# Kernel optimization log

Measured on AMD Instinct MI355X. Metric: run time of the kernel, lower is better.

The kernel has to match this reference:

```python
import jax, jax.numpy as jnp
import numpy as np

# Module hyperparameters (from init_kwargs)
LATENT = 1024
H = 16          # num query heads
HK = 4          # num key/value heads (GQA)
D = 64          # head_dim
CAUSAL = True
QKV_OUT = (3 * H + 2 * HK) * D  # 3584, as defined in the source module


def setup_inputs() -> dict:
    key = jax.random.key(0)
    k1, k2, k3 = jax.random.split(key, 3)
    B, S = 2, 2048
    x = jax.random.normal(k1, (B, S, LATENT), dtype=jnp.float32)
    # nn.Linear weights are [out_features, in_features]; scale like torch default init
    w_qkv = jax.random.normal(k2, (QKV_OUT, LATENT), dtype=jnp.float32) / np.sqrt(LATENT)
    w_out = jax.random.normal(k3, (LATENT, H * D), dtype=jnp.float32) / np.sqrt(H * D)
    return {"x": x, "w_qkv": w_qkv, "w_out": w_out}


def reference(x, w_qkv, w_out):
    B, S, _ = x.shape
    scale = 1.0 / np.sqrt(D).astype(np.float32)

    # Fused QKV projection: [B,S,(3H+2HK)*D]
    qkv = jnp.einsum('bsl,ol->bso', x, w_qkv)

    # Split: q takes H heads, k and v take HK heads each (GQA).
    # (The extra 2*H*D columns of the fused projection are allocated by the
    #  source module but unused by q/k/v, matching its layer sizing.)
    q = qkv[..., : H * D].reshape(B, S, H, D)
    k = qkv[..., H * D:(H + HK) * D].reshape(B, S, HK, D)
    v = qkv[..., (H + HK) * D:(H + 2 * HK) * D].reshape(B, S, HK, D)

    # Expand KV heads to match query heads (group factor H // HK)
    rep = H // HK
    k = jnp.repeat(k, rep, axis=2)  # [B,S,H,D]
    v = jnp.repeat(v, rep, axis=2)

    # Scaled dot-product attention
    scores = jnp.einsum('bshd,bthd->bhst', q, k) * scale  # [B,H,S,S]
    if CAUSAL:
        causal_mask = jnp.tril(jnp.ones((S, S), dtype=bool))
        scores = jnp.where(causal_mask, scores, jnp.finfo(scores.dtype).min)
    attn = jax.nn.softmax(scores, axis=-1)
    out = jnp.einsum('bhst,bthd->bshd', attn, v).reshape(B, S, H * D)

    # Output projection back to latent_size
    return jnp.einsum('bso,lo->bsl', out, w_out)
```

## Files before the change

### kernel.cpp

```cpp
#include <hip/hip_runtime.h>
#include <hip/hip_bf16.h>
#include <math.h>

typedef __attribute__((ext_vector_type(8))) short bf16x8;
typedef __attribute__((ext_vector_type(4))) float f32x4;
typedef unsigned short u16;
typedef unsigned int   u32;

#define DEVINL __device__ __forceinline__

DEVINL u16 f2bf(float x) {
    u32 u = __float_as_uint(x);
    u += 0x7fffu + ((u >> 16) & 1u);
    return (u16)(u >> 16);
}

DEVINL void gl_lds16(const void* g, void* s) {
    __builtin_amdgcn_global_load_lds(
        (const __attribute__((address_space(1))) u32*)g,
        (__attribute__((address_space(3))) u32*)s,
        16, 0, 0);
}

DEVINL f32x4 mfma16(bf16x8 a, bf16x8 b, f32x4 c) {
    return __builtin_amdgcn_mfma_f32_16x16x32_bf16(a, b, c, 0, 0, 0);
}

__global__ void cvt3(const float* __restrict__ x, const float* __restrict__ wq,
                     const float* __restrict__ wo,
                     u16* __restrict__ xb, u16* __restrict__ wqb, u16* __restrict__ wob) {
    int i = blockIdx.x * 256 + threadIdx.x;
    const float* s; u16* d; int j;
    if (i < 1048576)      { s = x;  d = xb;  j = i; }
    else if (i < 1441792) { s = wq; d = wqb; j = i - 1048576; }
    else                  { s = wo; d = wob; j = i - 1441792; }
    float4 v = ((const float4*)s)[j];
    ushort4 o;
    o.x = f2bf(v.x); o.y = f2bf(v.y); o.z = f2bf(v.z); o.w = f2bf(v.w);
    ((ushort4*)d)[j] = o;
}

template<int EP>
__launch_bounds__(256)
__global__ void gemm_bt(const u16* __restrict__ A, const u16* __restrict__ B,
                        const int N, const int K,
                        float* __restrict__ Cf,
                        u16* __restrict__ Qo, u16* __restrict__ Ko, u16* __restrict__ Vo)
{
    __shared__ __align__(16) u16 As[64 * 64];
    __shared__ __align__(16) u16 Bs[128 * 64];
    const int tid  = threadIdx.x;
    const int lane = tid & 63;
    const int quad = lane >> 4;
    const int lcol = lane & 15;
    const int w    = tid >> 6;
    const int wr   = w >> 1, wc = w & 1;
    const int lr   = lane >> 3;
    const int lc   = lane & 7;
    const int swst = lc ^ lr;
    const int rk   = lcol & 7;
    const int m0 = blockIdx.y * 64;
    const int n0 = blockIdx.x * 128;

    f32x4 acc[2][4];
    for (int mb = 0; mb < 2; mb++)
        for (int nb = 0; nb < 4; nb++)
            for (int i = 0; i < 4; i++) acc[mb][nb][i] = 0.f;

    const u16* Ap = A + (m0 + w * 16 + lr) * K + swst * 8;
    const u16* Bp = B + (n0 + w * 32 + lr) * K + swst * 8;

    for (int k0 = 0; k0 < K; k0 += 64) {
        gl_lds16(Ap + k0,         As + (w * 2 + 0) * 512);
        gl_lds16(Ap + 8 * K + k0, As + (w * 2 + 1) * 512);
        for (int g = 0; g < 4; g++)
            gl_lds16(Bp + g * 8 * K + k0, Bs + (w * 4 + g) * 512);
        __syncthreads();
        bf16x8 af[2][2], bfv[4][2];
        for (int ks = 0; ks < 2; ks++) {
            const int ch = ((ks * 4 + quad) ^ rk) * 8;
            for (int mb = 0; mb < 2; mb++)
                af[mb][ks] = *(const bf16x8*)&As[(wr * 32 + mb * 16 + lcol) * 64 + ch];
            for (int nb = 0; nb < 4; nb++)
                bfv[nb][ks] = *(const bf16x8*)&Bs[(wc * 64 + nb * 16 + lcol) * 64 + ch];
        }
        for (int ks = 0; ks < 2; ks++)
            for (int mb = 0; mb < 2; mb++)
                for (int nb = 0; nb < 4; nb++)
                    acc[mb][nb] = mfma16(af[mb][ks], bfv[nb][ks], acc[mb][nb]);
        __syncthreads();
    }

    if (EP == 0) {
        for (int mb = 0; mb < 2; mb++)
            for (int nb = 0; nb < 4; nb++) {
                int row = m0 + wr * 32 + mb * 16 + quad * 4;
                int col = n0 + wc * 64 + nb * 16 + lcol;
                for (int i = 0; i < 4; i++)
                    Cf[(row + i) * N + col] = acc[mb][nb][i];
            }
    } else {
        const float qsc = 0.18033688011112042f;
        for (int mb = 0; mb < 2; mb++)
            for (int nb = 0; nb < 4; nb++)
                for (int i = 0; i < 4; i++) {
                    int row = m0 + wr * 32 + mb * 16 + quad * 4 + i;
                    int col = n0 + wc * 64 + nb * 16 + lcol;
                    int bb = row >> 11, ss = row & 2047;
                    if (col < 1024) {
                        int hh = col >> 6, dd = col & 63;
                        Qo[((bb * 16 + hh) * 2048 + ss) * 64 + dd] = f2bf(acc[mb][nb][i] * qsc);
                    } else if (col < 1280) {
                        int c = col - 1024, hh = c >> 6, dd = c & 63;
                        Ko[((bb * 4 + hh) * 2048 + ss) * 64 + dd] = f2bf(acc[mb][nb][i]);
                    } else {
                        int c = col - 1280, hh = c >> 6, dd = c & 63;
                        Vo[((bb * 4 + hh) * 64 + dd) * 2048 + ss] = f2bf(acc[mb][nb][i]);
                    }
                }
    }
}

__launch_bounds__(256)
__global__ void attn_kernel(const u16* __restrict__ Qg, const u16* __restrict__ Kg,
                            const u16* __restrict__ Vtg, u16* __restrict__ Og)
{
    __shared__ __align__(16) u16 Ks[2][64 * 64];
    __shared__ __align__(16) u16 Vs[2][64 * 64];
    __shared__ __align__(16) u16 Ps[64 * 64];

    const int tid  = threadIdx.x;
    const int lane = tid & 63;
    const int w    = tid >> 6;
    const int quad = lane >> 4;
    const int lcol = lane & 15;
    const int lr   = lane >> 3;
    const int lc   = lane & 7;
    const int swst = lc ^ lr;
    const int rk   = lcol & 7;

    const int p  = blockIdx.x;
    const int h  = blockIdx.y;
    const int b  = blockIdx.z;
    const int hk = h >> 2;

    const u16* Qp = Qg  + (b * 16 + h) * 2048 * 64;
    const u16* Kp = Kg  + (b * 4 + hk) * 2048 * 64;
    const u16* Vp = Vtg + (b * 4 + hk) * 64 * 2048;

    for (int pass = 0; pass < 2; pass++) {
        const int qi = pass ? (31 - p) : p;
        const int q0 = qi * 64;
        const int nt = qi + 1;

        bf16x8 aqr[2];
        for (int ks = 0; ks < 2; ks++)
            aqr[ks] = *(const bf16x8*)(Qp + (q0 + w * 16 + lcol) * 64 + ks * 32 + quad * 8);

        for (int j = 0; j < 2; j++) {
            const int r = w * 16 + j * 8 + lr;
            gl_lds16(Kp + r * 64 + swst * 8,   &Ks[0][w * 1024 + j * 512]);
            gl_lds16(Vp + r * 2048 + swst * 8, &Vs[0][w * 1024 + j * 512]);
        }

        f32x4 o[4];
        float l_p[4];
        for (int db = 0; db < 4; db++)
            for (int i = 0; i < 4; i++) o[db][i] = 0.f;
        for (int i = 0; i < 4; i++) l_p[i] = 0.f;

        __syncthreads();

        for (int ti = 0; ti < nt; ti++) {
            const int cur = ti & 1;
            if (ti + 1 < nt) {
                const int nb = cur ^ 1;
                const int t0n = (ti + 1) * 64;
                for (int j = 0; j < 2; j++) {
                    const int r = w * 16 + j * 8 + lr;
                    gl_lds16(Kp + (t0n + r) * 64 + swst * 8, &Ks[nb][w * 1024 + j * 512]);
                    gl_lds16(Vp + r * 2048 + t0n + swst * 8, &Vs[nb][w * 1024 + j * 512]);
                }
            }

            f32x4 s[4];
            for (int cb = 0; cb < 4; cb++)
                for (int i = 0; i < 4; i++) s[cb][i] = 0.f;
            for (int ks = 0; ks < 2; ks++) {
                const int chq = ((ks * 4 + quad) ^ rk) * 8;
                for (int cb = 0; cb < 4; cb++) {
                    bf16x8 bk = *(const bf16x8*)&Ks[cur][(cb * 16 + lcol) * 64 + chq];
                    s[cb] = mfma16(aqr[ks], bk, s[cb]);
                }
            }

            if (ti == nt - 1) {
                for (int cb = 0; cb < 4; cb++)
                    for (int i = 0; i < 4; i++) {
                        const bool masked = (cb * 16 + lcol) > (w * 16 + quad * 4 + i);
                        s[cb][i] = masked ? -INFINITY : s[cb][i];
                    }
            }

            for (int cb = 0; cb < 4; cb++)
                for (int i = 0; i < 4; i++) {
                    const float pv = exp2f(s[cb][i]);
                    s[cb][i] = pv;
                    l_p[i] += pv;
                }

            for (int cb = 0; cb < 4; cb++)
                for (int i = 0; i < 4; i++) {
                    const int rl = quad * 4 + i;
                    const int cc = cb * 2 + (lcol >> 3);
                    Ps[(w * 16 + rl) * 64 + ((cc ^ (rl & 7)) << 3) + lc] =
                        (u16)(__float_as_uint(s[cb][i]) >> 16);
                }

            for (int kt = 0; kt < 2; kt++) {
                const int chp = ((kt * 4 + quad) ^ rk) * 8;
                bf16x8 ap = *(const bf16x8*)&Ps[(w * 16 + lcol) * 64 + chp];
                for (int db = 0; db < 4; db++) {
                    bf16x8 bv = *(const bf16x8*)&Vs[cur][(db * 16 + lcol) * 64 + chp];
                    o[db] = mfma16(ap, bv, o[db]);
                }
            }
            __syncthreads();
        }

        for (int i = 0; i < 4; i++) {
            float l = l_p[i];
            for (int x = 1; x < 16; x <<= 1) l += __shfl_xor(l, x);
            const float inv = 1.0f / l;
            const int srow = q0 + w * 16 + quad * 4 + i;
            for (int db = 0; db < 4; db++)
                Og[(b * 2048 + srow) * 1024 + h * 64 + db * 16 + lcol] = f2bf(o[db][i] * inv);
        }
    }
}

extern "C" void kernel_launch(void* const* d_in, const int* in_sizes, int n_in,
                              void* d_out, int out_size, void* d_ws, size_t ws_size,
                              hipStream_t stream) {
    const float* x     = (const float*)d_in[0];
    const float* w_qkv = (const float*)d_in[1];
    const float* w_out = (const float*)d_in[2];
    float* out = (float*)d_out;
    char* ws = (char*)d_ws;

    u16* xb  = (u16*)(ws);
    u16* wqb = (u16*)(ws + 8  * 1024 * 1024);
    u16* wob = (u16*)(ws + 11 * 1024 * 1024);
    u16* qb  = (u16*)(ws + 13 * 1024 * 1024);
    u16* kb  = (u16*)(ws + 21 * 1024 * 1024);
    u16* vtb = (u16*)(ws + 23 * 1024 * 1024);
    u16* aob = (u16*)(ws);

    cvt3<<<6656, 256, 0, stream>>>(x, w_qkv, w_out, xb, wqb, wob);

    gemm_bt<1><<<dim3(12, 64), 256, 0, stream>>>(xb, wqb, 1536, 1024,
                                                 nullptr, qb, kb, vtb);
    attn_kernel<<<dim3(16, 16, 2), 256, 0, stream>>>(qb, kb, vtb, aob);
    gemm_bt<0><<<dim3(8, 64), 256, 0, stream>>>(aob, wob, 1024, 1024,
                                                out, nullptr, nullptr, nullptr);
}
```

Baseline: 170.2 us.

## Double-buffer GEMM LDS tiles with register prefetch and narrow output-projection tiles

```diff
diff --git a/kernel.cpp b/kernel.cpp
--- a/kernel.cpp
+++ b/kernel.cpp
@@ -40,15 +40,16 @@
     ((ushort4*)d)[j] = o;
 }
 
-template<int EP>
+template<int BN, int EP>
 __launch_bounds__(256)
-__global__ void gemm_bt(const u16* __restrict__ A, const u16* __restrict__ B,
+__global__ void gemm_rp(const u16* __restrict__ A, const u16* __restrict__ B,
                         const int N, const int K,
                         float* __restrict__ Cf,
                         u16* __restrict__ Qo, u16* __restrict__ Ko, u16* __restrict__ Vo)
 {
-    __shared__ __align__(16) u16 As[64 * 64];
-    __shared__ __align__(16) u16 Bs[128 * 64];
+    constexpr int NB = BN / 32;
+    __shared__ __align__(16) u16 As[2][64 * 64];
+    __shared__ __align__(16) u16 Bs[2][BN * 64];
     const int tid  = threadIdx.x;
     const int lane = tid & 63;
     const int quad = lane >> 4;
@@ -60,52 +61,69 @@
     const int swst = lc ^ lr;
     const int rk   = lcol & 7;
     const int m0 = blockIdx.y * 64;
-    const int n0 = blockIdx.x * 128;
-
-    f32x4 acc[2][4];
+    const int n0 = blockIdx.x * BN;
+
+    f32x4 acc[2][NB];
     for (int mb = 0; mb < 2; mb++)
-        for (int nb = 0; nb < 4; nb++)
+        for (int nb = 0; nb < NB; nb++)
             for (int i = 0; i < 4; i++) acc[mb][nb][i] = 0.f;
 
     const u16* Ap = A + (m0 + w * 16 + lr) * K + swst * 8;
-    const u16* Bp = B + (n0 + w * 32 + lr) * K + swst * 8;
-
+    const u16* Bp = B + (n0 + w * (BN / 4) + lr) * K + swst * 8;
+
+    bf16x8 areg[2], breg[NB];
+    for (int j = 0; j < 2; j++)  areg[j] = *(const bf16x8*)(Ap + j * 8 * K);
+    for (int g = 0; g < NB; g++) breg[g] = *(const bf16x8*)(Bp + g * 8 * K);
+    for (int j = 0; j < 2; j++)
+        *(bf16x8*)&As[0][(w * 16 + j * 8 + lr) * 64 + lc * 8] = areg[j];
+    for (int g = 0; g < NB; g++)
+        *(bf16x8*)&Bs[0][(w * (BN / 4) + g * 8 + lr) * 64 + lc * 8] = breg[g];
+    __syncthreads();
+
+    int cur = 0;
     for (int k0 = 0; k0 < K; k0 += 64) {
-        gl_lds16(Ap + k0,         As + (w * 2 + 0) * 512);
-        gl_lds16(Ap + 8 * K + k0, As + (w * 2 + 1) * 512);
-        for (int g = 0; g < 4; g++)
-            gl_lds16(Bp + g * 8 * K + k0, Bs + (w * 4 + g) * 512);
-        __syncthreads();
-        bf16x8 af[2][2], bfv[4][2];
+        const bool more = (k0 + 64 < K);
+        if (more) {
+            for (int j = 0; j < 2; j++)  areg[j] = *(const bf16x8*)(Ap + j * 8 * K + k0 + 64);
+            for (int g = 0; g < NB; g++) breg[g] = *(const bf16x8*)(Bp + g * 8 * K + k0 + 64);
+        }
+        bf16x8 af[2][2], bfv[NB][2];
         for (int ks = 0; ks < 2; ks++) {
             const int ch = ((ks * 4 + quad) ^ rk) * 8;
             for (int mb = 0; mb < 2; mb++)
-                af[mb][ks] = *(const bf16x8*)&As[(wr * 32 + mb * 16 + lcol) * 64 + ch];
-            for (int nb = 0; nb < 4; nb++)
-                bfv[nb][ks] = *(const bf16x8*)&Bs[(wc * 64 + nb * 16 + lcol) * 64 + ch];
+                af[mb][ks] = *(const bf16x8*)&As[cur][(wr * 32 + mb * 16 + lcol) * 64 + ch];
+            for (int nb = 0; nb < NB; nb++)
+                bfv[nb][ks] = *(const bf16x8*)&Bs[cur][(wc * (BN / 2) + nb * 16 + lcol) * 64 + ch];
         }
         for (int ks = 0; ks < 2; ks++)
             for (int mb = 0; mb < 2; mb++)
-                for (int nb = 0; nb < 4; nb++)
+                for (int nb = 0; nb < NB; nb++)
                     acc[mb][nb] = mfma16(af[mb][ks], bfv[nb][ks], acc[mb][nb]);
+        if (more) {
+            for (int j = 0; j < 2; j++)
+                *(bf16x8*)&As[cur ^ 1][(w * 16 + j * 8 + lr) * 64 + lc * 8] = areg[j];
+            for (int g = 0; g < NB; g++)
+                *(bf16x8*)&Bs[cur ^ 1][(w * (BN / 4) + g * 8 + lr) * 64 + lc * 8] = breg[g];
+        }
         __syncthreads();
+        cur ^= 1;
     }
 
     if (EP == 0) {
         for (int mb = 0; mb < 2; mb++)
-            for (int nb = 0; nb < 4; nb++) {
+            for (int nb = 0; nb < NB; nb++) {
                 int row = m0 + wr * 32 + mb * 16 + quad * 4;
-                int col = n0 + wc * 64 + nb * 16 + lcol;
+                int col = n0 + wc * (BN / 2) + nb * 16 + lcol;
                 for (int i = 0; i < 4; i++)
                     Cf[(row + i) * N + col] = acc[mb][nb][i];
             }
     } else {
         const float qsc = 0.18033688011112042f;
         for (int mb = 0; mb < 2; mb++)
-            for (int nb = 0; nb < 4; nb++)
+            for (int nb = 0; nb < NB; nb++)
                 for (int i = 0; i < 4; i++) {
                     int row = m0 + wr * 32 + mb * 16 + quad * 4 + i;
-                    int col = n0 + wc * 64 + nb * 16 + lcol;
+                    int col = n0 + wc * (BN / 2) + nb * 16 + lcol;
                     int bb = row >> 11, ss = row & 2047;
                     if (col < 1024) {
                         int hh = col >> 6, dd = col & 63;
@@ -258,9 +276,9 @@
 
     cvt3<<<6656, 256, 0, stream>>>(x, w_qkv, w_out, xb, wqb, wob);
 
-    gemm_bt<1><<<dim3(12, 64), 256, 0, stream>>>(xb, wqb, 1536, 1024,
-                                                 nullptr, qb, kb, vtb);
+    gemm_rp<128, 1><<<dim3(12, 64), 256, 0, stream>>>(xb, wqb, 1536, 1024,
+                                                      nullptr, qb, kb, vtb);
     attn_kernel<<<dim3(16, 16, 2), 256, 0, stream>>>(qb, kb, vtb, aob);
-    gemm_bt<0><<<dim3(8, 64), 256, 0, stream>>>(aob, wob, 1024, 1024,
-                                                out, nullptr, nullptr, nullptr);
-}
+    gemm_rp<64, 0><<<dim3(16, 64), 256, 0, stream>>>(aob, wob, 1024, 1024,
+                                                     out, nullptr, nullptr, nullptr);
+}
```

Result: no change. 166.9 us (-2.0%).

## Use two-wave blocks for GEMMs and 32-row query tiles for attention

Applied to the files above, without the earlier changes.

```diff
diff --git a/kernel.cpp b/kernel.cpp
--- a/kernel.cpp
+++ b/kernel.cpp
@@ -41,8 +41,8 @@
 }
 
 template<int EP>
-__launch_bounds__(256)
-__global__ void gemm_bt(const u16* __restrict__ A, const u16* __restrict__ B,
+__launch_bounds__(128)
+__global__ void gemm_w2(const u16* __restrict__ A, const u16* __restrict__ B,
                         const int N, const int K,
                         float* __restrict__ Cf,
                         u16* __restrict__ Qo, u16* __restrict__ Ko, u16* __restrict__ Vo)
@@ -54,7 +54,6 @@
     const int quad = lane >> 4;
     const int lcol = lane & 15;
     const int w    = tid >> 6;
-    const int wr   = w >> 1, wc = w & 1;
     const int lr   = lane >> 3;
     const int lc   = lane & 7;
     const int swst = lc ^ lr;
@@ -62,50 +61,50 @@
     const int m0 = blockIdx.y * 64;
     const int n0 = blockIdx.x * 128;
 
-    f32x4 acc[2][4];
-    for (int mb = 0; mb < 2; mb++)
+    f32x4 acc[4][4];
+    for (int mb = 0; mb < 4; mb++)
         for (int nb = 0; nb < 4; nb++)
             for (int i = 0; i < 4; i++) acc[mb][nb][i] = 0.f;
 
-    const u16* Ap = A + (m0 + w * 16 + lr) * K + swst * 8;
-    const u16* Bp = B + (n0 + w * 32 + lr) * K + swst * 8;
+    const u16* Ap = A + (m0 + w * 32 + lr) * K + swst * 8;
+    const u16* Bp = B + (n0 + w * 64 + lr) * K + swst * 8;
 
     for (int k0 = 0; k0 < K; k0 += 64) {
-        gl_lds16(Ap + k0,         As + (w * 2 + 0) * 512);
-        gl_lds16(Ap + 8 * K + k0, As + (w * 2 + 1) * 512);
-        for (int g = 0; g < 4; g++)
-            gl_lds16(Bp + g * 8 * K + k0, Bs + (w * 4 + g) * 512);
+        for (int j = 0; j < 4; j++)
+            gl_lds16(Ap + j * 8 * K + k0, As + (w * 32 + j * 8) * 64);
+        for (int j = 0; j < 8; j++)
+            gl_lds16(Bp + j * 8 * K + k0, Bs + (w * 64 + j * 8) * 64);
         __syncthreads();
-        bf16x8 af[2][2], bfv[4][2];
+        bf16x8 af[4][2], bfv[4][2];
         for (int ks = 0; ks < 2; ks++) {
             const int ch = ((ks * 4 + quad) ^ rk) * 8;
-            for (int mb = 0; mb < 2; mb++)
-                af[mb][ks] = *(const bf16x8*)&As[(wr * 32 + mb * 16 + lcol) * 64 + ch];
+            for (int mb = 0; mb < 4; mb++)
+                af[mb][ks] = *(const bf16x8*)&As[(mb * 16 + lcol) * 64 + ch];
             for (int nb = 0; nb < 4; nb++)
-                bfv[nb][ks] = *(const bf16x8*)&Bs[(wc * 64 + nb * 16 + lcol) * 64 + ch];
+                bfv[nb][ks] = *(const bf16x8*)&Bs[(w * 64 + nb * 16 + lcol) * 64 + ch];
         }
         for (int ks = 0; ks < 2; ks++)
-            for (int mb = 0; mb < 2; mb++)
+            for (int mb = 0; mb < 4; mb++)
                 for (int nb = 0; nb < 4; nb++)
                     acc[mb][nb] = mfma16(af[mb][ks], bfv[nb][ks], acc[mb][nb]);
         __syncthreads();
     }
 
     if (EP == 0) {
-        for (int mb = 0; mb < 2; mb++)
+        for (int mb = 0; mb < 4; mb++)
             for (int nb = 0; nb < 4; nb++) {
-                int row = m0 + wr * 32 + mb * 16 + quad * 4;
-                int col = n0 + wc * 64 + nb * 16 + lcol;
+                int row = m0 + mb * 16 + quad * 4;
+                int col = n0 + w * 64 + nb * 16 + lcol;
                 for (int i = 0; i < 4; i++)
                     Cf[(row + i) * N + col] = acc[mb][nb][i];
             }
     } else {
         const float qsc = 0.18033688011112042f;
-        for (int mb = 0; mb < 2; mb++)
+        for (int mb = 0; mb < 4; mb++)
             for (int nb = 0; nb < 4; nb++)
                 for (int i = 0; i < 4; i++) {
-                    int row = m0 + wr * 32 + mb * 16 + quad * 4 + i;
-                    int col = n0 + wc * 64 + nb * 16 + lcol;
+                    int row = m0 + mb * 16 + quad * 4 + i;
+                    int col = n0 + w * 64 + nb * 16 + lcol;
                     int bb = row >> 11, ss = row & 2047;
                     if (col < 1024) {
                         int hh = col >> 6, dd = col & 63;
@@ -121,13 +120,13 @@
     }
 }
 
-__launch_bounds__(256)
+__launch_bounds__(128)
 __global__ void attn_kernel(const u16* __restrict__ Qg, const u16* __restrict__ Kg,
                             const u16* __restrict__ Vtg, u16* __restrict__ Og)
 {
     __shared__ __align__(16) u16 Ks[2][64 * 64];
     __shared__ __align__(16) u16 Vs[2][64 * 64];
-    __shared__ __align__(16) u16 Ps[64 * 64];
+    __shared__ __align__(16) u16 Ps[32 * 64];
 
     const int tid  = threadIdx.x;
     const int lane = tid & 63;
@@ -149,18 +148,18 @@
     const u16* Vp = Vtg + (b * 4 + hk) * 64 * 2048;
 
     for (int pass = 0; pass < 2; pass++) {
-        const int qi = pass ? (31 - p) : p;
-        const int q0 = qi * 64;
-        const int nt = qi + 1;
+        const int qi = pass ? (63 - p) : p;
+        const int q0 = qi * 32;
+        const int nt = (qi >> 1) + 1;
 
         bf16x8 aqr[2];
         for (int ks = 0; ks < 2; ks++)
             aqr[ks] = *(const bf16x8*)(Qp + (q0 + w * 16 + lcol) * 64 + ks * 32 + quad * 8);
 
-        for (int j = 0; j < 2; j++) {
-            const int r = w * 16 + j * 8 + lr;
-            gl_lds16(Kp + r * 64 + swst * 8,   &Ks[0][w * 1024 + j * 512]);
-            gl_lds16(Vp + r * 2048 + swst * 8, &Vs[0][w * 1024 + j * 512]);
+        for (int j = 0; j < 4; j++) {
+            const int r = w * 32 + j * 8 + lr;
+            gl_lds16(Kp + r * 64 + swst * 8,   &Ks[0][(w * 32 + j * 8) * 64]);
+            gl_lds16(Vp + r * 2048 + swst * 8, &Vs[0][(w * 32 + j * 8) * 64]);
         }
 
         f32x4 o[4];
@@ -176,10 +175,10 @@
             if (ti + 1 < nt) {
                 const int nb = cur ^ 1;
                 const int t0n = (ti + 1) * 64;
-                for (int j = 0; j < 2; j++) {
-                    const int r = w * 16 + j * 8 + lr;
-                    gl_lds16(Kp + (t0n + r) * 64 + swst * 8, &Ks[nb][w * 1024 + j * 512]);
-                    gl_lds16(Vp + r * 2048 + t0n + swst * 8, &Vs[nb][w * 1024 + j * 512]);
+                for (int j = 0; j < 4; j++) {
+                    const int r = w * 32 + j * 8 + lr;
+                    gl_lds16(Kp + (t0n + r) * 64 + swst * 8, &Ks[nb][(w * 32 + j * 8) * 64]);
+                    gl_lds16(Vp + r * 2048 + t0n + swst * 8, &Vs[nb][(w * 32 + j * 8) * 64]);
                 }
             }
 
@@ -195,10 +194,12 @@
             }
 
             if (ti == nt - 1) {
+                const int t0 = ti * 64;
                 for (int cb = 0; cb < 4; cb++)
                     for (int i = 0; i < 4; i++) {
-                        const bool masked = (cb * 16 + lcol) > (w * 16 + quad * 4 + i);
-                        s[cb][i] = masked ? -INFINITY : s[cb][i];
+                        const int rg = q0 + w * 16 + quad * 4 + i;
+                        const int cg = t0 + cb * 16 + lcol;
+                        s[cb][i] = (cg > rg) ? -INFINITY : s[cb][i];
                     }
             }
 
@@ -258,9 +259,9 @@
 
     cvt3<<<6656, 256, 0, stream>>>(x, w_qkv, w_out, xb, wqb, wob);
 
-    gemm_bt<1><<<dim3(12, 64), 256, 0, stream>>>(xb, wqb, 1536, 1024,
+    gemm_w2<1><<<dim3(12, 64), 128, 0, stream>>>(xb, wqb, 1536, 1024,
                                                  nullptr, qb, kb, vtb);
-    attn_kernel<<<dim3(16, 16, 2), 256, 0, stream>>>(qb, kb, vtb, aob);
-    gemm_bt<0><<<dim3(8, 64), 256, 0, stream>>>(aob, wob, 1024, 1024,
+    attn_kernel<<<dim3(32, 16, 2), 128, 0, stream>>>(qb, kb, vtb, aob);
+    gemm_w2<0><<<dim3(8, 64), 128, 0, stream>>>(aob, wob, 1024, 1024,
                                                 out, nullptr, nullptr, nullptr);
 }
```

Result: slower. 180.9 us (+6.3%).

## Use 32x32 MFMA with two-wave blocks in projection GEMMs

Applied to the files above, without the earlier changes.

```diff
diff --git a/kernel.cpp b/kernel.cpp
--- a/kernel.cpp
+++ b/kernel.cpp
@@ -4,6 +4,7 @@
 
 typedef __attribute__((ext_vector_type(8))) short bf16x8;
 typedef __attribute__((ext_vector_type(4))) float f32x4;
+typedef __attribute__((ext_vector_type(16))) float f32x16;
 typedef unsigned short u16;
 typedef unsigned int   u32;
 
@@ -24,6 +25,9 @@
 
 DEVINL f32x4 mfma16(bf16x8 a, bf16x8 b, f32x4 c) {
     return __builtin_amdgcn_mfma_f32_16x16x32_bf16(a, b, c, 0, 0, 0);
+}
+DEVINL f32x16 mfma32(bf16x8 a, bf16x8 b, f32x16 c) {
+    return __builtin_amdgcn_mfma_f32_32x32x16_bf16(a, b, c, 0, 0, 0);
 }
 
 __global__ void cvt3(const float* __restrict__ x, const float* __restrict__ wq,
@@ -41,8 +45,8 @@
 }
 
 template<int EP>
-__launch_bounds__(256)
-__global__ void gemm_bt(const u16* __restrict__ A, const u16* __restrict__ B,
+__launch_bounds__(128)
+__global__ void gemm_w2(const u16* __restrict__ A, const u16* __restrict__ B,
                         const int N, const int K,
                         float* __restrict__ Cf,
                         u16* __restrict__ Qo, u16* __restrict__ Ko, u16* __restrict__ Vo)
@@ -51,71 +55,70 @@
     __shared__ __align__(16) u16 Bs[128 * 64];
     const int tid  = threadIdx.x;
     const int lane = tid & 63;
-    const int quad = lane >> 4;
-    const int lcol = lane & 15;
     const int w    = tid >> 6;
-    const int wr   = w >> 1, wc = w & 1;
+    const int l31  = lane & 31;
+    const int half = lane >> 5;
     const int lr   = lane >> 3;
     const int lc   = lane & 7;
     const int swst = lc ^ lr;
-    const int rk   = lcol & 7;
+    const int rk   = lane & 7;
     const int m0 = blockIdx.y * 64;
     const int n0 = blockIdx.x * 128;
 
-    f32x4 acc[2][4];
-    for (int mb = 0; mb < 2; mb++)
-        for (int nb = 0; nb < 4; nb++)
-            for (int i = 0; i < 4; i++) acc[mb][nb][i] = 0.f;
-
-    const u16* Ap = A + (m0 + w * 16 + lr) * K + swst * 8;
-    const u16* Bp = B + (n0 + w * 32 + lr) * K + swst * 8;
+    f32x16 acc[2][2];
+    for (int mf = 0; mf < 2; mf++)
+        for (int nf = 0; nf < 2; nf++)
+            for (int i = 0; i < 16; i++) acc[mf][nf][i] = 0.f;
+
+    const u16* Ap = A + (m0 + w * 32 + lr) * K + swst * 8;
+    const u16* Bp = B + (n0 + w * 64 + lr) * K + swst * 8;
 
     for (int k0 = 0; k0 < K; k0 += 64) {
-        gl_lds16(Ap + k0,         As + (w * 2 + 0) * 512);
-        gl_lds16(Ap + 8 * K + k0, As + (w * 2 + 1) * 512);
-        for (int g = 0; g < 4; g++)
-            gl_lds16(Bp + g * 8 * K + k0, Bs + (w * 4 + g) * 512);
+        for (int j = 0; j < 4; j++)
+            gl_lds16(Ap + j * 8 * K + k0, As + (w * 32 + j * 8) * 64);
+        for (int j = 0; j < 8; j++)
+            gl_lds16(Bp + j * 8 * K + k0, Bs + (w * 64 + j * 8) * 64);
         __syncthreads();
-        bf16x8 af[2][2], bfv[4][2];
-        for (int ks = 0; ks < 2; ks++) {
-            const int ch = ((ks * 4 + quad) ^ rk) * 8;
-            for (int mb = 0; mb < 2; mb++)
-                af[mb][ks] = *(const bf16x8*)&As[(wr * 32 + mb * 16 + lcol) * 64 + ch];
-            for (int nb = 0; nb < 4; nb++)
-                bfv[nb][ks] = *(const bf16x8*)&Bs[(wc * 64 + nb * 16 + lcol) * 64 + ch];
-        }
-        for (int ks = 0; ks < 2; ks++)
-            for (int mb = 0; mb < 2; mb++)
-                for (int nb = 0; nb < 4; nb++)
-                    acc[mb][nb] = mfma16(af[mb][ks], bfv[nb][ks], acc[mb][nb]);
+        bf16x8 af[2][4], bfv[2][4];
+        for (int ks = 0; ks < 4; ks++) {
+            const int ch = ((ks * 2 + half) ^ rk) * 8;
+            for (int mf = 0; mf < 2; mf++)
+                af[mf][ks] = *(const bf16x8*)&As[(mf * 32 + l31) * 64 + ch];
+            for (int nf = 0; nf < 2; nf++)
+                bfv[nf][ks] = *(const bf16x8*)&Bs[(w * 64 + nf * 32 + l31) * 64 + ch];
+        }
+        for (int ks = 0; ks < 4; ks++)
+            for (int mf = 0; mf < 2; mf++)
+                for (int nf = 0; nf < 2; nf++)
+                    acc[mf][nf] = mfma32(af[mf][ks], bfv[nf][ks], acc[mf][nf]);
         __syncthreads();
     }
 
     if (EP == 0) {
-        for (int mb = 0; mb < 2; mb++)
-            for (int nb = 0; nb < 4; nb++) {
-                int row = m0 + wr * 32 + mb * 16 + quad * 4;
-                int col = n0 + wc * 64 + nb * 16 + lcol;
-                for (int i = 0; i < 4; i++)
-                    Cf[(row + i) * N + col] = acc[mb][nb][i];
-            }
+        for (int mf = 0; mf < 2; mf++)
+            for (int nf = 0; nf < 2; nf++)
+                for (int r = 0; r < 16; r++) {
+                    int row = m0 + mf * 32 + (r & 3) + 8 * (r >> 2) + 4 * half;
+                    int col = n0 + w * 64 + nf * 32 + l31;
+                    Cf[row * N + col] = acc[mf][nf][r];
+                }
     } else {
         const float qsc = 0.18033688011112042f;
-        for (int mb = 0; mb < 2; mb++)
-            for (int nb = 0; nb < 4; nb++)
-                for (int i = 0; i < 4; i++) {
-                    int row = m0 + wr * 32 + mb * 16 + quad * 4 + i;
-                    int col = n0 + wc * 64 + nb * 16 + lcol;
+        for (int mf = 0; mf < 2; mf++)
+            for (int nf = 0; nf < 2; nf++)
+                for (int r = 0; r < 16; r++) {
+                    int row = m0 + mf * 32 + (r & 3) + 8 * (r >> 2) + 4 * half;
+                    int col = n0 + w * 64 + nf * 32 + l31;
                     int bb = row >> 11, ss = row & 2047;
                     if (col < 1024) {
                         int hh = col >> 6, dd = col & 63;
-                        Qo[((bb * 16 + hh) * 2048 + ss) * 64 + dd] = f2bf(acc[mb][nb][i] * qsc);
+                        Qo[((bb * 16 + hh) * 2048 + ss) * 64 + dd] = f2bf(acc[mf][nf][r] * qsc);
                     } else if (col < 1280) {
                         int c = col - 1024, hh = c >> 6, dd = c & 63;
-                        Ko[((bb * 4 + hh) * 2048 + ss) * 64 + dd] = f2bf(acc[mb][nb][i]);
+                        Ko[((bb * 4 + hh) * 2048 + ss) * 64 + dd] = f2bf(acc[mf][nf][r]);
                     } else {
                         int c = col - 1280, hh = c >> 6, dd = c & 63;
-                        Vo[((bb * 4 + hh) * 64 + dd) * 2048 + ss] = f2bf(acc[mb][nb][i]);
+                        Vo[((bb * 4 + hh) * 64 + dd) * 2048 + ss] = f2bf(acc[mf][nf][r]);
                     }
                 }
     }
@@ -258,9 +261,9 @@
 
     cvt3<<<6656, 256, 0, stream>>>(x, w_qkv, w_out, xb, wqb, wob);
 
-    gemm_bt<1><<<dim3(12, 64), 256, 0, stream>>>(xb, wqb, 1536, 1024,
+    gemm_w2<1><<<dim3(12, 64), 128, 0, stream>>>(xb, wqb, 1536, 1024,
                                                  nullptr, qb, kb, vtb);
     attn_kernel<<<dim3(16, 16, 2), 256, 0, stream>>>(qb, kb, vtb, aob);
-    gemm_bt<0><<<dim3(8, 64), 256, 0, stream>>>(aob, wob, 1024, 1024,
+    gemm_w2<0><<<dim3(8, 64), 128, 0, stream>>>(aob, wob, 1024, 1024,
                                                 out, nullptr, nullptr, nullptr);
 }
```

Measured after the change: 175.6 us. 3.2% more time.
